# Kernel tuning notes

Hardware: AMD Instinct MI355X
Metric: run time of the kernel (lower is better)

Reference implementation:

```python
import jax, jax.numpy as jnp
import numpy as np
from jax.scipy.special import logsumexp

EPSILON = 0.1
MAX_ITER = 200


def setup_inputs() -> dict:
    key = jax.random.key(0)
    bs, n, m = 32, 2048, 512
    C = jax.random.uniform(key, (bs, n, m), dtype=jnp.float32)  # nonnegative cost
    mu = jnp.full((1, n, 1), 1.0 / n, dtype=jnp.float32)  # uniform row marginal
    nu = jnp.full((1, 1, m), 1.0 / m, dtype=jnp.float32)  # uniform col marginal
    return {"C": C, "mu": mu, "nu": nu}


def _sinkhorn_plain(C, mu, nu, eps, max_iter):
    bs, n, m = C.shape
    G = jnp.exp(-C / eps)
    u0 = jnp.ones((bs, n, 1), C.dtype)
    v0 = jnp.ones((bs, 1, m), C.dtype) / m

    def body(carry, _):
        u, v = carry
        u = mu / jnp.sum(G * v, axis=-1, keepdims=True)
        v = nu / jnp.sum(G * u, axis=-2, keepdims=True)
        return (u, v), None

    (u, v), _ = jax.lax.scan(body, (u0, v0), None, length=max_iter)
    return u * G * v


def _sinkhorn_stablized(C, mu, nu, eps, max_iter):
    bs, n, m = C.shape
    f0 = jnp.zeros((bs, n, 1), C.dtype)
    g0 = jnp.zeros((bs, 1, m), C.dtype)
    eps_log_mu = eps * jnp.log(mu)
    eps_log_nu = eps * jnp.log(nu)

    def body(carry, _):
        f, g = carry
        f = -eps * logsumexp(-(C - g) / eps, axis=-1, keepdims=True) + eps_log_mu
        g = -eps * logsumexp(-(C - f) / eps, axis=-2, keepdims=True) + eps_log_nu
        return (f, g), None

    (f, g), _ = jax.lax.scan(body, (f0, g0), None, length=max_iter)
    return jnp.exp((-C + f + g) / eps)


def reference(C, mu, nu):
    # TopKFunc.forward: plain Sinkhorn when epsilon / C.max() > 0.01,
    # otherwise log-domain stabilized Sinkhorn.
    use_plain = EPSILON / jnp.max(C) > 0.01
    return jax.lax.cond(
        use_plain,
        lambda c: _sinkhorn_plain(c, mu, nu, EPSILON, MAX_ITER),
        lambda c: _sinkhorn_stablized(c, mu, nu, EPSILON, MAX_ITER),
        C,
    )
```

## Files before the change

### kernel.cpp

```cpp
#include <hip/hip_runtime.h>
#include <hip/hip_fp16.h>


namespace {
constexpr int BS   = 32;
constexpr int N    = 2048;
constexpr int M    = 512;
constexpr int NBLK = 16;
constexpr int RPB  = N / NBLK;
constexpr int ITERS = 200;
constexpr int BLOCK = 1024;
constexpr int WAVES = BLOCK / 64;
constexpr int CPAD  = M + 8;
constexpr float MU_C = 1.0f / (float)N;
constexpr float NU_C = 1.0f / (float)M;
constexpr int PCNT = BS * NBLK * M;
}

__global__ __launch_bounds__(256) void build_G_kernel(const float* __restrict__ C,
                                                      __half* __restrict__ G) {
    int idx = blockIdx.x * 256 + threadIdx.x;
    int stride = gridDim.x * 256;
    int total4 = BS * N * M / 4;
    for (int k = idx; k < total4; k += stride) {
        float4 c = reinterpret_cast<const float4*>(C)[k];
        union { uint2 u2; __half2 h2[2]; } pk;
        pk.h2[0] = __floats2half2_rn(expf(-10.0f * c.x), expf(-10.0f * c.y));
        pk.h2[1] = __floats2half2_rn(expf(-10.0f * c.z), expf(-10.0f * c.w));
        reinterpret_cast<uint2*>(G)[k] = pk.u2;
    }
}

template <bool RECOMPUTE>
__device__ __forceinline__ void load_gf(const __half* __restrict__ G,
                                        const float* __restrict__ C,
                                        size_t base, float gf[8]) {
    if constexpr (RECOMPUTE) {
        float4 c0 = *reinterpret_cast<const float4*>(C + base);
        float4 c1 = *reinterpret_cast<const float4*>(C + base + 4);
        gf[0] = __expf(-10.0f * c0.x); gf[1] = __expf(-10.0f * c0.y);
        gf[2] = __expf(-10.0f * c0.z); gf[3] = __expf(-10.0f * c0.w);
        gf[4] = __expf(-10.0f * c1.x); gf[5] = __expf(-10.0f * c1.y);
        gf[6] = __expf(-10.0f * c1.z); gf[7] = __expf(-10.0f * c1.w);
    } else {
        union { uint4 u4; __half2 h2[4]; } pk;
        pk.u4 = *reinterpret_cast<const uint4*>(G + base);
        float2 f;
        f = __half22float2(pk.h2[0]); gf[0] = f.x; gf[1] = f.y;
        f = __half22float2(pk.h2[1]); gf[2] = f.x; gf[3] = f.y;
        f = __half22float2(pk.h2[2]); gf[4] = f.x; gf[5] = f.y;
        f = __half22float2(pk.h2[3]); gf[6] = f.x; gf[7] = f.y;
    }
}

template <bool RECOMPUTE>
__global__ __launch_bounds__(BLOCK) void sinkhorn_iter_kernel(
    const __half* __restrict__ G, const float* __restrict__ C,
    const float* __restrict__ P_in, float* __restrict__ P_out,
    float* __restrict__ u_out, int first)
{
    __shared__ float v_s[M];
    __shared__ float colacc[WAVES][CPAD];
    const int wg  = blockIdx.x;
    const int b   = wg / NBLK;
    const int blk = wg % NBLK;
    const int tid = threadIdx.x;

    if (first) {
        if (tid < M) v_s[tid] = NU_C;
    } else {
        if (tid < M) {
            const float* p = P_in + (size_t)b * NBLK * M + tid;
            float s = 0.0f;
            #pragma unroll
            for (int k = 0; k < NBLK; ++k) s += p[(size_t)k * M];
            v_s[tid] = NU_C / s;
        }
    }
    __syncthreads();

    const int wave = tid >> 6;
    const int lane = tid & 63;

    float vreg[8];
    #pragma unroll
    for (int k = 0; k < 8; ++k) vreg[k] = v_s[lane * 8 + k];

    float cacc[8] = {0.f, 0.f, 0.f, 0.f, 0.f, 0.f, 0.f, 0.f};
    const int row0 = blk * RPB;

    #pragma unroll 2
    for (int it = 0; it < RPB / WAVES; ++it) {
        const int row = row0 + it * WAVES + wave;
        const size_t base = ((size_t)b * N + row) * M + lane * 8;
        float gf[8];
        load_gf<RECOMPUTE>(G, C, base, gf);
        float dot = 0.0f;
        #pragma unroll
        for (int k = 0; k < 8; ++k) dot += gf[k] * vreg[k];
        #pragma unroll
        for (int off = 32; off > 0; off >>= 1) dot += __shfl_xor(dot, off, 64);
        const float u = MU_C / dot;
        if (lane == 0) u_out[(size_t)b * N + row] = u;
        #pragma unroll
        for (int k = 0; k < 8; ++k) cacc[k] += gf[k] * u;
    }

    #pragma unroll
    for (int k = 0; k < 8; ++k) colacc[wave][lane * 8 + k] = cacc[k];
    __syncthreads();
    if (tid < M) {
        float s = 0.0f;
        #pragma unroll
        for (int w = 0; w < WAVES; ++w) s += colacc[w][tid];
        P_out[(size_t)wg * M + tid] = s;
    }
}

template <bool RECOMPUTE>
__global__ __launch_bounds__(BLOCK) void sinkhorn_out_kernel(
    const __half* __restrict__ G, const float* __restrict__ C,
    const float* __restrict__ P_in, const float* __restrict__ u_in,
    float* __restrict__ out)
{
    __shared__ float v_s[M];
    const int wg  = blockIdx.x;
    const int b   = wg / NBLK;
    const int blk = wg % NBLK;
    const int tid = threadIdx.x;

    if (tid < M) {
        const float* p = P_in + (size_t)b * NBLK * M + tid;
        float s = 0.0f;
        #pragma unroll
        for (int k = 0; k < NBLK; ++k) s += p[(size_t)k * M];
        v_s[tid] = NU_C / s;
    }
    __syncthreads();

    const int wave = tid >> 6;
    const int lane = tid & 63;
    float vreg[8];
    #pragma unroll
    for (int k = 0; k < 8; ++k) vreg[k] = v_s[lane * 8 + k];

    const int row0 = blk * RPB;
    #pragma unroll 2
    for (int it = 0; it < RPB / WAVES; ++it) {
        const int row = row0 + it * WAVES + wave;
        const size_t base = ((size_t)b * N + row) * M + lane * 8;
        const float u = u_in[(size_t)b * N + row];
        float gf[8];
        load_gf<RECOMPUTE>(G, C, base, gf);
        float4 o0, o1;
        o0.x = u * gf[0] * vreg[0]; o0.y = u * gf[1] * vreg[1];
        o0.z = u * gf[2] * vreg[2]; o0.w = u * gf[3] * vreg[3];
        o1.x = u * gf[4] * vreg[4]; o1.y = u * gf[5] * vreg[5];
        o1.z = u * gf[6] * vreg[6]; o1.w = u * gf[7] * vreg[7];
        *reinterpret_cast<float4*>(out + base)     = o0;
        *reinterpret_cast<float4*>(out + base + 4) = o1;
    }
}

extern "C" void kernel_launch(void* const* d_in, const int* in_sizes, int n_in,
                              void* d_out, int out_size, void* d_ws, size_t ws_size,
                              hipStream_t stream) {
    const float* C = (const float*)d_in[0];
    float* out = (float*)d_out;
    char* ws = (char*)d_ws;

    const size_t G_bytes = (size_t)BS * N * M * sizeof(__half);
    const size_t P_bytes = (size_t)2 * PCNT * sizeof(float);
    const bool primary = ws_size >= G_bytes + P_bytes + (size_t)BS * N * sizeof(float);

    __half* G;
    float*  P;
    float*  u;
    if (primary) {
        G = (__half*)ws;
        P = (float*)(ws + G_bytes);
        u = P + 2 * PCNT;
        build_G_kernel<<<4096, 256, 0, stream>>>(C, G);
    } else {
        G = nullptr;
        P = (float*)ws;
        u = P + 2 * PCNT;
    }

    const int grid = BS * NBLK;
    for (int t = 0; t < ITERS; ++t) {
        const float* Pin  = P + ((t + 1) & 1) * PCNT;
        float*       Pout = P + (t & 1) * PCNT;
        if (primary)
            sinkhorn_iter_kernel<false><<<grid, BLOCK, 0, stream>>>(G, C, Pin, Pout, u, t == 0);
        else
            sinkhorn_iter_kernel<true><<<grid, BLOCK, 0, stream>>>(G, C, Pin, Pout, u, t == 0);
    }
    const float* Pfin = P + ((ITERS - 1) & 1) * PCNT;
    if (primary)
        sinkhorn_out_kernel<false><<<grid, BLOCK, 0, stream>>>(G, C, Pfin, u, out);
    else
        sinkhorn_out_kernel<true><<<grid, BLOCK, 0, stream>>>(G, C, Pfin, u, out);
}
```

Measured before the change: 3.059 ms.

## Run all Sinkhorn iterations in one persistent cooperative kernel with register-resident G

Replaces the 200 per-iteration kernel launches with a single cooperative persistent kernel of 256 workgroups. Each workgroup keeps its slice of G (fp16) in registers for the whole run and synchronizes with the other workgroups of its batch through a global atomic barrier. This removes launch overhead and the repeated global reads of G every iteration. It also uses DPP/permlane wave reductions and swizzled LDS indexing. The risks are register pressure from holding 128 packed values per thread, the need for cooperative-launch residency, and spin-barrier latency, with a fallback to the old multi-launch path if the launch fails.

```diff
diff --git a/kernel.cpp b/kernel.cpp
--- a/kernel.cpp
+++ b/kernel.cpp
@@ -3,19 +3,200 @@
 
 
 namespace {
-constexpr int BS   = 32;
-constexpr int N    = 2048;
-constexpr int M    = 512;
-constexpr int NBLK = 16;
-constexpr int RPB  = N / NBLK;
+constexpr int BS = 32;
+constexpr int N  = 2048;
+constexpr int M  = 512;
 constexpr int ITERS = 200;
-constexpr int BLOCK = 1024;
-constexpr int WAVES = BLOCK / 64;
-constexpr int CPAD  = M + 8;
-constexpr float MU_C = 1.0f / (float)N;
-constexpr float NU_C = 1.0f / (float)M;
-constexpr int PCNT = BS * NBLK * M;
-}
+constexpr float MU_C = 1.0f / 2048.0f;
+constexpr float NU_C = 1.0f / 512.0f;
+
+constexpr int PB     = 8;
+constexpr int PGRID  = BS * PB;
+constexpr int PBLOCK = 1024;
+constexpr int PWAVES = PBLOCK / 64;
+constexpr int PRPB   = N / PB;
+constexpr int PRPW   = PRPB / PWAVES;
+constexpr int PCPAD  = M + 8;
+constexpr int PPCNT  = BS * PB * M;
+constexpr int BARSTRIDE = 16;
+
+constexpr int NBLK   = 16;
+constexpr int RPB    = N / NBLK;
+constexpr int FBLOCK = 1024;
+constexpr int FWAVES = FBLOCK / 64;
+constexpr int FCPAD  = M + 8;
+constexpr int FPCNT  = BS * NBLK * M;
+}
+
+
+__device__ __forceinline__ int swz(int j) {
+    int c = j >> 2;
+    c ^= (c >> 3) & 7;
+    return (c << 2) | (j & 3);
+}
+
+__device__ __forceinline__ void unpack8(const unsigned* gq, float* gf) {
+    #pragma unroll
+    for (int k = 0; k < 4; ++k) {
+        union { unsigned u; __half2 h; } q; q.u = gq[k];
+        float2 f = __half22float2(q.h);
+        gf[2 * k] = f.x; gf[2 * k + 1] = f.y;
+    }
+}
+
+__device__ __forceinline__ float wave_sum64(float x) {
+    x += __int_as_float(__builtin_amdgcn_update_dpp(0, __float_as_int(x), 0x121, 0xF, 0xF, true));
+    x += __int_as_float(__builtin_amdgcn_update_dpp(0, __float_as_int(x), 0x122, 0xF, 0xF, true));
+    x += __int_as_float(__builtin_amdgcn_update_dpp(0, __float_as_int(x), 0x124, 0xF, 0xF, true));
+    x += __int_as_float(__builtin_amdgcn_update_dpp(0, __float_as_int(x), 0x128, 0xF, 0xF, true));
+#if __has_builtin(__builtin_amdgcn_permlane16_swap)
+    {
+        auto r = __builtin_amdgcn_permlane16_swap(__float_as_int(x), __float_as_int(x), false, false);
+        x = __int_as_float(r[0]) + __int_as_float(r[1]);
+    }
+#else
+    x += __int_as_float(__builtin_amdgcn_ds_swizzle(__float_as_int(x), 0x401F));
+#endif
+#if __has_builtin(__builtin_amdgcn_permlane32_swap)
+    {
+        auto r = __builtin_amdgcn_permlane32_swap(__float_as_int(x), __float_as_int(x), false, false);
+        x = __int_as_float(r[0]) + __int_as_float(r[1]);
+    }
+#else
+    x += __shfl_xor(x, 32, 64);
+#endif
+    return x;
+}
+
+
+__global__ __launch_bounds__(512) void bar_init_kernel(unsigned* __restrict__ bar) {
+    bar[threadIdx.x] = 0u;
+}
+
+__global__ __launch_bounds__(PBLOCK, 4) void sinkhorn_persist(
+    const float* __restrict__ C, float* __restrict__ P,
+    float* __restrict__ u_ws, unsigned* __restrict__ bar,
+    float* __restrict__ out)
+{
+    __shared__ __align__(16) float v_s[M];
+    __shared__ __align__(16) float colacc[PWAVES][PCPAD];
+
+    const int wg   = blockIdx.x;
+    const int b    = wg & (BS - 1);
+    const int blk  = wg >> 5;
+    const int tid  = threadIdx.x;
+    const int wave = tid >> 6;
+    const int lane = tid & 63;
+    const int row0 = blk * PRPB;
+
+    const int stid = swz(tid & (M - 1));
+    float* const vp0 = &v_s[swz(lane * 8)];
+    float* const vp1 = &v_s[swz(lane * 8 + 4)];
+    float* const cp0 = &colacc[wave][swz(lane * 8)];
+    float* const cp1 = &colacc[wave][swz(lane * 8 + 4)];
+
+    unsigned g[PRPW][4];
+    #pragma unroll
+    for (int it = 0; it < PRPW; ++it) {
+        const int row = row0 + it * PWAVES + wave;
+        const size_t base = ((size_t)b * N + row) * M + lane * 8;
+        const float4 c0 = *reinterpret_cast<const float4*>(C + base);
+        const float4 c1 = *reinterpret_cast<const float4*>(C + base + 4);
+        union { unsigned u; __half2 h; } q;
+        q.h = __floats2half2_rn(expf(-10.0f * c0.x), expf(-10.0f * c0.y)); g[it][0] = q.u;
+        q.h = __floats2half2_rn(expf(-10.0f * c0.z), expf(-10.0f * c0.w)); g[it][1] = q.u;
+        q.h = __floats2half2_rn(expf(-10.0f * c1.x), expf(-10.0f * c1.y)); g[it][2] = q.u;
+        q.h = __floats2half2_rn(expf(-10.0f * c1.z), expf(-10.0f * c1.w)); g[it][3] = q.u;
+    }
+
+    unsigned* const mybar = bar + b * BARSTRIDE;
+
+    #pragma unroll 1
+    for (int t = 0; t < ITERS; ++t) {
+        if (tid < M) {
+            float vv;
+            if (t == 0) {
+                vv = NU_C;
+            } else {
+                const float* p = P + (size_t)((t + 1) & 1) * PPCNT + (size_t)b * PB * M + tid;
+                float s = p[0];
+                #pragma unroll
+                for (int k = 1; k < PB; ++k) s += p[(size_t)k * M];
+                vv = NU_C / s;
+            }
+            v_s[stid] = vv;
+        }
+        __syncthreads();
+
+        const float4 v0 = *reinterpret_cast<const float4*>(vp0);
+        const float4 v1 = *reinterpret_cast<const float4*>(vp1);
+
+        float4 ca0 = {0.f, 0.f, 0.f, 0.f}, ca1 = {0.f, 0.f, 0.f, 0.f};
+        #pragma unroll
+        for (int it = 0; it < PRPW; ++it) {
+            float gf[8];
+            unpack8(g[it], gf);
+            float dot = gf[0] * v0.x + gf[1] * v0.y + gf[2] * v0.z + gf[3] * v0.w
+                      + gf[4] * v1.x + gf[5] * v1.y + gf[6] * v1.z + gf[7] * v1.w;
+            dot = wave_sum64(dot);
+            const float u = MU_C / dot;
+            if (t == ITERS - 1 && lane == 0)
+                u_ws[(size_t)b * N + (row0 + it * PWAVES + wave)] = u;
+            ca0.x += gf[0] * u; ca0.y += gf[1] * u; ca0.z += gf[2] * u; ca0.w += gf[3] * u;
+            ca1.x += gf[4] * u; ca1.y += gf[5] * u; ca1.z += gf[6] * u; ca1.w += gf[7] * u;
+        }
+
+        *reinterpret_cast<float4*>(cp0) = ca0;
+        *reinterpret_cast<float4*>(cp1) = ca1;
+        __syncthreads();
+        if (tid < M) {
+            float s = colacc[0][stid];
+            #pragma unroll
+            for (int w = 1; w < PWAVES; ++w) s += colacc[w][stid];
+            P[(size_t)(t & 1) * PPCNT + ((size_t)b * PB + blk) * M + tid] = s;
+        }
+
+        __syncthreads();
+        if (tid == 0) {
+            __builtin_amdgcn_fence(__ATOMIC_RELEASE, "agent");
+            __hip_atomic_fetch_add(mybar, 1u, __ATOMIC_RELAXED, __HIP_MEMORY_SCOPE_AGENT);
+            const unsigned tgt = (unsigned)(t + 1) * (unsigned)PB;
+            while (__hip_atomic_load(mybar, __ATOMIC_RELAXED, __HIP_MEMORY_SCOPE_AGENT) < tgt)
+                __builtin_amdgcn_s_sleep(1);
+            __builtin_amdgcn_fence(__ATOMIC_ACQUIRE, "agent");
+        }
+        __syncthreads();
+    }
+
+    if (tid < M) {
+        const float* p = P + (size_t)((ITERS - 1) & 1) * PPCNT + (size_t)b * PB * M + tid;
+        float s = p[0];
+        #pragma unroll
+        for (int k = 1; k < PB; ++k) s += p[(size_t)k * M];
+        v_s[stid] = NU_C / s;
+    }
+    __syncthreads();
+    {
+        const float4 v0 = *reinterpret_cast<const float4*>(vp0);
+        const float4 v1 = *reinterpret_cast<const float4*>(vp1);
+        #pragma unroll
+        for (int it = 0; it < PRPW; ++it) {
+            const int row = row0 + it * PWAVES + wave;
+            const size_t base = ((size_t)b * N + row) * M + lane * 8;
+            const float u = u_ws[(size_t)b * N + row];
+            float gf[8];
+            unpack8(g[it], gf);
+            float4 o0, o1;
+            o0.x = u * gf[0] * v0.x; o0.y = u * gf[1] * v0.y;
+            o0.z = u * gf[2] * v0.z; o0.w = u * gf[3] * v0.w;
+            o1.x = u * gf[4] * v1.x; o1.y = u * gf[5] * v1.y;
+            o1.z = u * gf[6] * v1.z; o1.w = u * gf[7] * v1.w;
+            *reinterpret_cast<float4*>(out + base)     = o0;
+            *reinterpret_cast<float4*>(out + base + 4) = o1;
+        }
+    }
+}
+
 
 __global__ __launch_bounds__(256) void build_G_kernel(const float* __restrict__ C,
                                                       __half* __restrict__ G) {
@@ -54,13 +235,13 @@
 }
 
 template <bool RECOMPUTE>
-__global__ __launch_bounds__(BLOCK) void sinkhorn_iter_kernel(
+__global__ __launch_bounds__(FBLOCK) void sinkhorn_iter_kernel(
     const __half* __restrict__ G, const float* __restrict__ C,
     const float* __restrict__ P_in, float* __restrict__ P_out,
     float* __restrict__ u_out, int first)
 {
     __shared__ float v_s[M];
-    __shared__ float colacc[WAVES][CPAD];
+    __shared__ float colacc[FWAVES][FCPAD];
     const int wg  = blockIdx.x;
     const int b   = wg / NBLK;
     const int blk = wg % NBLK;
@@ -90,8 +271,8 @@
     const int row0 = blk * RPB;
 
     #pragma unroll 2
-    for (int it = 0; it < RPB / WAVES; ++it) {
-        const int row = row0 + it * WAVES + wave;
+    for (int it = 0; it < RPB / FWAVES; ++it) {
+        const int row = row0 + it * FWAVES + wave;
         const size_t base = ((size_t)b * N + row) * M + lane * 8;
         float gf[8];
         load_gf<RECOMPUTE>(G, C, base, gf);
@@ -112,13 +293,13 @@
     if (tid < M) {
         float s = 0.0f;
         #pragma unroll
-        for (int w = 0; w < WAVES; ++w) s += colacc[w][tid];
+        for (int w = 0; w < FWAVES; ++w) s += colacc[w][tid];
         P_out[(size_t)wg * M + tid] = s;
     }
 }
 
 template <bool RECOMPUTE>
-__global__ __launch_bounds__(BLOCK) void sinkhorn_out_kernel(
+__global__ __launch_bounds__(FBLOCK) void sinkhorn_out_kernel(
     const __half* __restrict__ G, const float* __restrict__ C,
     const float* __restrict__ P_in, const float* __restrict__ u_in,
     float* __restrict__ out)
@@ -146,8 +327,8 @@
 
     const int row0 = blk * RPB;
     #pragma unroll 2
-    for (int it = 0; it < RPB / WAVES; ++it) {
-        const int row = row0 + it * WAVES + wave;
+    for (int it = 0; it < RPB / FWAVES; ++it) {
+        const int row = row0 + it * FWAVES + wave;
         const size_t base = ((size_t)b * N + row) * M + lane * 8;
         const float u = u_in[(size_t)b * N + row];
         float gf[8];
@@ -162,15 +343,35 @@
     }
 }
 
+
 extern "C" void kernel_launch(void* const* d_in, const int* in_sizes, int n_in,
                               void* d_out, int out_size, void* d_ws, size_t ws_size,
                               hipStream_t stream) {
+    (void)in_sizes; (void)n_in; (void)out_size;
     const float* C = (const float*)d_in[0];
     float* out = (float*)d_out;
     char* ws = (char*)d_ws;
 
+    {
+        float* P2      = (float*)ws;
+        float* u2      = P2 + (size_t)2 * PPCNT;
+        unsigned* bar  = (unsigned*)(u2 + (size_t)BS * N);
+        const size_t need = ((size_t)2 * PPCNT + (size_t)BS * N) * sizeof(float)
+                          + (size_t)BS * BARSTRIDE * sizeof(unsigned);
+        if (ws_size >= need) {
+            hipLaunchKernelGGL(bar_init_kernel, dim3(1), dim3(BS * BARSTRIDE), 0, stream, bar);
+            const float* Ca = C; float* Pa = P2; float* ua = u2; unsigned* ba = bar; float* oa = out;
+            void* args[5] = { &Ca, &Pa, &ua, &ba, &oa };
+            hipError_t e = hipLaunchCooperativeKernel((const void*)sinkhorn_persist,
+                                                      dim3(PGRID), dim3(PBLOCK),
+                                                      args, 0, stream);
+            if (e == hipSuccess) return;
+            (void)hipGetLastError();
+        }
+    }
+
     const size_t G_bytes = (size_t)BS * N * M * sizeof(__half);
-    const size_t P_bytes = (size_t)2 * PCNT * sizeof(float);
+    const size_t P_bytes = (size_t)2 * FPCNT * sizeof(float);
     const bool primary = ws_size >= G_bytes + P_bytes + (size_t)BS * N * sizeof(float);
 
     __half* G;
@@ -179,26 +380,26 @@
     if (primary) {
         G = (__half*)ws;
         P = (float*)(ws + G_bytes);
-        u = P + 2 * PCNT;
+        u = P + 2 * FPCNT;
         build_G_kernel<<<4096, 256, 0, stream>>>(C, G);
     } else {
         G = nullptr;
         P = (float*)ws;
-        u = P + 2 * PCNT;
+        u = P + 2 * FPCNT;
     }
 
     const int grid = BS * NBLK;
     for (int t = 0; t < ITERS; ++t) {
-        const float* Pin  = P + ((t + 1) & 1) * PCNT;
-        float*       Pout = P + (t & 1) * PCNT;
+        const float* Pin  = P + ((t + 1) & 1) * FPCNT;
+        float*       Pout = P + (t & 1) * FPCNT;
         if (primary)
-            sinkhorn_iter_kernel<false><<<grid, BLOCK, 0, stream>>>(G, C, Pin, Pout, u, t == 0);
+            sinkhorn_iter_kernel<false><<<grid, FBLOCK, 0, stream>>>(G, C, Pin, Pout, u, t == 0);
         else
-            sinkhorn_iter_kernel<true><<<grid, BLOCK, 0, stream>>>(G, C, Pin, Pout, u, t == 0);
-    }
-    const float* Pfin = P + ((ITERS - 1) & 1) * PCNT;
+            sinkhorn_iter_kernel<true><<<grid, FBLOCK, 0, stream>>>(G, C, Pin, Pout, u, t == 0);
+    }
+    const float* Pfin = P + ((ITERS - 1) & 1) * FPCNT;
     if (primary)
-        sinkhorn_out_kernel<false><<<grid, BLOCK, 0, stream>>>(G, C, Pfin, u, out);
+        sinkhorn_out_kernel<false><<<grid, FBLOCK, 0, stream>>>(G, C, Pfin, u, out);
     else
-        sinkhorn_out_kernel<true><<<grid, BLOCK, 0, stream>>>(G, C, Pfin, u, out);
-}
+        sinkhorn_out_kernel<true><<<grid, FBLOCK, 0, stream>>>(G, C, Pfin, u, out);
+}
```

Result: slower. 5.273 ms (+72.4%).
